# Kernel tuning notes

Hardware: AMD Instinct MI355X
Metric: run time of the kernel (lower is better)

Reference implementation:

```python
import jax, jax.numpy as jnp
import numpy as np

THRESH = 0.1  # Hardshrink lambda from init_kwargs


def setup_inputs() -> dict:
    key = jax.random.key(0)
    k1, k2, k3 = jax.random.split(key, 3)
    m, n, N = 64, 256, 131072
    phi = jax.random.normal(k1, (m, n), dtype=jnp.float32)
    X = jax.random.normal(k2, (n, N), dtype=jnp.float32)
    Y = jax.random.normal(k3, (m, N), dtype=jnp.float32)
    step = jnp.ones((1,), dtype=jnp.float32)  # learnable ISTA step size
    return {"phi": phi, "X": X, "Y": Y, "step": step, "idx": 100000}


def reference(phi, X, Y, step, idx):
    # The torch module updates column idx, then columns 0..idx-1, each with
    #   X[:, i] = hardshrink(X[:, i] + step * phi.T @ (Y[:, i] - phi @ X[:, i]))
    # (note: -(-1)*step == +step). Columns are independent and each column
    # reads only its own pre-update value, so the per-column loop is exactly
    # equivalent to two batched GEMMs over the prefix X[:, :idx+1] plus one
    # fused hard-threshold pass.
    k = idx + 1  # number of updated columns (idx is a static Python int)
    cols = X[:, :k]                       # [n, k]
    resid = Y[:, :k] - phi @ cols         # [m, k]
    upd = cols + step[0] * (phi.T @ resid)  # [n, k] gradient step
    upd = jnp.where(jnp.abs(upd) > THRESH, upd, jnp.zeros((), upd.dtype))
    X = X.at[:, :k].set(upd)
    return phi, X
```

## Files before the change

### kernel.cpp

```cpp
#include <hip/hip_runtime.h>
#include <math.h>

constexpr int M   = 64;
constexpr int NR  = 256;
constexpr int KK  = NR + M;
constexpr int NC  = 131072;
constexpr int BN  = 64;
constexpr float THR = 0.1f;

typedef __bf16 bf16x8 __attribute__((ext_vector_type(8)));
typedef float  f32x4  __attribute__((ext_vector_type(4)));

static __device__ __forceinline__ unsigned short f2bf(float f) {
    unsigned int u = __float_as_uint(f);
    u += 0x7FFFu + ((u >> 16) & 1u);
    return (unsigned short)(u >> 16);
}

__global__ __launch_bounds__(256)
void k_copy_phi(const float* __restrict__ phi, float* __restrict__ out)
{
    int i = blockIdx.x * 256 + threadIdx.x;
    out[i] = phi[i];
}

__global__ __launch_bounds__(256)
void k_prep(const float* __restrict__ phi, const float* __restrict__ step,
            unsigned short* __restrict__ A)
{
    __shared__ float ph[M * NR];
    const int i = blockIdx.x, j = threadIdx.x;
    for (int t = j; t < M * NR; t += 256) ph[t] = phi[t];
    __syncthreads();
    const float s = step[0];
    float d = 0.f;
    #pragma unroll
    for (int m = 0; m < M; ++m)
        d = fmaf(ph[m * NR + i], ph[m * NR + j], d);
    float w = ((i == j) ? 1.f : 0.f) - s * d;
    A[i * KK + j] = f2bf(w);
    if (j < M) A[i * KK + NR + j] = f2bf(s * ph[j * NR + i]);
}

__global__ __launch_bounds__(256, 3)
void k_gemm(const unsigned short* __restrict__ A,
            const float* __restrict__ X,
            const float* __restrict__ Y,
            const int*   __restrict__ idxp,
            float* __restrict__ outX)
{
    const int k   = idxp[0] + 1;
    const int n0  = blockIdx.x * BN;
    const int tid = threadIdx.x;

    if (n0 >= k) {
        const int c4 = tid & 15, rg = tid >> 4;
        #pragma unroll 4
        for (int r = rg; r < NR; r += 16) {
            const float4* src = (const float4*)(X + (size_t)r * NC + n0);
            float4*       dst = (float4*)(outX + (size_t)r * NC + n0);
            dst[c4] = src[c4];
        }
        return;
    }

    __shared__ unsigned int Bu32[10 * 2560 / 2];

    {
        const int n = tid & 63, slot = tid >> 6;
        for (int p = slot; p < KK / 2; p += 4) {
            const int r = p << 1;
            const float* s0 = (r < NR) ? (X + (size_t)r * NC)
                                       : (Y + (size_t)(r - NR) * NC);
            const float* s1 = (r < NR) ? (X + (size_t)(r + 1) * NC)
                                       : (Y + (size_t)(r + 1 - NR) * NC);
            float v0 = s0[n0 + n], v1 = s1[n0 + n];
            const int kb = r >> 5, kl = r & 31;
            Bu32[(kb * 2560 + n * 40 + kl) >> 1] =
                (unsigned int)f2bf(v0) | ((unsigned int)f2bf(v1) << 16);
        }
    }
    __syncthreads();

    const int lane = tid & 63, wave = tid >> 6;
    const int quad = lane >> 4, nlo = lane & 15;
    const int mbase = wave * 64;

    f32x4 acc[4][4];
    #pragma unroll
    for (int mt = 0; mt < 4; ++mt)
        #pragma unroll
        for (int nt = 0; nt < 4; ++nt)
            acc[mt][nt] = (f32x4){0.f, 0.f, 0.f, 0.f};

    const unsigned short* Abase = A + (size_t)(mbase + nlo) * KK + quad * 8;
    const unsigned int*   Bbase = Bu32 + ((nlo * 40 + quad * 8) >> 1);

    #pragma unroll 2
    for (int kb = 0; kb < 10; ++kb) {
        bf16x8 afr[4], bfr[4];
        #pragma unroll
        for (int mt = 0; mt < 4; ++mt)
            afr[mt] = *(const bf16x8*)(Abase + (size_t)mt * 16 * KK + kb * 32);
        #pragma unroll
        for (int nt = 0; nt < 4; ++nt)
            bfr[nt] = *(const bf16x8*)(Bbase + (kb * 2560 + nt * 16 * 40) / 2);
        #pragma unroll
        for (int mt = 0; mt < 4; ++mt)
            #pragma unroll
            for (int nt = 0; nt < 4; ++nt)
                acc[mt][nt] = __builtin_amdgcn_mfma_f32_16x16x32_bf16(
                    afr[mt], bfr[nt], acc[mt][nt], 0, 0, 0);
    }

    const bool boundary = (n0 + BN > k);
    #pragma unroll
    for (int mt = 0; mt < 4; ++mt) {
        #pragma unroll
        for (int nt = 0; nt < 4; ++nt) {
            const int col = n0 + nt * 16 + nlo;
            #pragma unroll
            for (int reg = 0; reg < 4; ++reg) {
                const int row = mbase + mt * 16 + quad * 4 + reg;
                float v = acc[mt][nt][reg];
                v = (fabsf(v) > THR) ? v : 0.f;
                if (boundary && col >= k) v = X[(size_t)row * NC + col];
                outX[(size_t)row * NC + col] = v;
            }
        }
    }
}

extern "C" void kernel_launch(void* const* d_in, const int* in_sizes, int n_in,
                              void* d_out, int out_size, void* d_ws, size_t ws_size,
                              hipStream_t stream)
{
    const float* phi  = (const float*)d_in[0];
    const float* X    = (const float*)d_in[1];
    const float* Y    = (const float*)d_in[2];
    const float* step = (const float*)d_in[3];
    const int*   idx  = (const int*)d_in[4];
    float* out = (float*)d_out;
    unsigned short* A = (unsigned short*)d_ws;

    k_copy_phi<<<(M * NR) / 256, 256, 0, stream>>>(phi, out);
    k_prep<<<NR, 256, 0, stream>>>(phi, step, A);
    k_gemm<<<NC / BN, 256, 0, stream>>>(A, X, Y, idx, out + M * NR);
}
```

Before: 322.9 us.

## Pre-swizzle A into fragment order, vectorize B staging, XOR-swizzle LDS, prefetch A

The prep kernel now writes the fused operator matrix in MFMA fragment order, so each lane loads contiguous 16-byte A fragments and the next k-block's A fragments can be prefetched into registers. B staging switches to float4 global loads that are held in registers and then written to an XOR-swizzled LDS layout, which is meant to avoid bank conflicts. The launch-bounds occupancy target rises from 3 to 4, and the copy loop is fully unrolled. The cost is higher register pressure from the 20 held float4 values plus the prefetched fragments, which may spill under the tighter occupancy bound.

Result: faster. 299.8 us (-7.1%).

```diff
diff --git a/kernel.cpp b/kernel.cpp
--- a/kernel.cpp
+++ b/kernel.cpp
@@ -15,6 +15,12 @@
     unsigned int u = __float_as_uint(f);
     u += 0x7FFFu + ((u >> 16) & 1u);
     return (unsigned short)(u >> 16);
+}
+
+static __device__ __forceinline__ int a_off(int i, int kk) {
+    const int wave = i >> 6, mt = (i >> 4) & 3, nlo = i & 15;
+    const int kb = kk >> 5, quad = (kk >> 3) & 3, j = kk & 7;
+    return (((wave * 10 + kb) * 4 + mt) << 9) + ((quad * 16 + nlo) << 3) + j;
 }
 
 __global__ __launch_bounds__(256)
@@ -38,11 +44,11 @@
     for (int m = 0; m < M; ++m)
         d = fmaf(ph[m * NR + i], ph[m * NR + j], d);
     float w = ((i == j) ? 1.f : 0.f) - s * d;
-    A[i * KK + j] = f2bf(w);
-    if (j < M) A[i * KK + NR + j] = f2bf(s * ph[j * NR + i]);
+    A[a_off(i, j)] = f2bf(w);
+    if (j < M) A[a_off(i, NR + j)] = f2bf(s * ph[j * NR + i]);
 }
 
-__global__ __launch_bounds__(256, 3)
+__global__ __launch_bounds__(256, 4)
 void k_gemm(const unsigned short* __restrict__ A,
             const float* __restrict__ X,
             const float* __restrict__ Y,
@@ -55,7 +61,7 @@
 
     if (n0 >= k) {
         const int c4 = tid & 15, rg = tid >> 4;
-        #pragma unroll 4
+        #pragma unroll
         for (int r = rg; r < NR; r += 16) {
             const float4* src = (const float4*)(X + (size_t)r * NC + n0);
             float4*       dst = (float4*)(outX + (size_t)r * NC + n0);
@@ -64,27 +70,41 @@
         return;
     }
 
-    __shared__ unsigned int Bu32[10 * 2560 / 2];
+    __shared__ unsigned int Bu32[10 * 4096 / 4];
 
-    {
-        const int n = tid & 63, slot = tid >> 6;
-        for (int p = slot; p < KK / 2; p += 4) {
-            const int r = p << 1;
-            const float* s0 = (r < NR) ? (X + (size_t)r * NC)
-                                       : (Y + (size_t)(r - NR) * NC);
-            const float* s1 = (r < NR) ? (X + (size_t)(r + 1) * NC)
-                                       : (Y + (size_t)(r + 1 - NR) * NC);
-            float v0 = s0[n0 + n], v1 = s1[n0 + n];
-            const int kb = r >> 5, kl = r & 31;
-            Bu32[(kb * 2560 + n * 40 + kl) >> 1] =
-                (unsigned int)f2bf(v0) | ((unsigned int)f2bf(v1) << 16);
+    const int c4 = tid & 15, rg = tid >> 4;
+    const int lane = tid & 63, wave = tid >> 6;
+    const int quad = lane >> 4, nlo = lane & 15;
+
+    f32x4 v0[10], v1[10];
+    #pragma unroll
+    for (int it = 0; it < 10; ++it) {
+        const int r0 = 32 * it + 2 * rg;
+        const float *s0, *s1;
+        if (r0 < NR) { s0 = X + (size_t)r0 * NC;        s1 = X + (size_t)(r0 + 1) * NC; }
+        else         { s0 = Y + (size_t)(r0 - NR) * NC; s1 = Y + (size_t)(r0 + 1 - NR) * NC; }
+        v0[it] = *(const f32x4*)(s0 + n0 + 4 * c4);
+        v1[it] = *(const f32x4*)(s1 + n0 + 4 * c4);
+    }
+
+    const unsigned short* Abase = A + ((wave * 40) << 9) + (lane << 3);
+    bf16x8 a_cur[4], a_nxt[4];
+    #pragma unroll
+    for (int mt = 0; mt < 4; ++mt)
+        a_cur[mt] = *(const bf16x8*)(Abase + (mt << 9));
+
+    #pragma unroll
+    for (int it = 0; it < 10; ++it) {
+        const int kl2 = 4 * rg;
+        #pragma unroll
+        for (int c = 0; c < 4; ++c) {
+            const int n = 4 * c4 + c;
+            const int byteoff = (it * 4096 + n * 64 + kl2) ^ ((n & 14) << 3);
+            Bu32[byteoff >> 2] =
+                (unsigned int)f2bf(v0[it][c]) | ((unsigned int)f2bf(v1[it][c]) << 16);
         }
     }
     __syncthreads();
-
-    const int lane = tid & 63, wave = tid >> 6;
-    const int quad = lane >> 4, nlo = lane & 15;
-    const int mbase = wave * 64;
 
     f32x4 acc[4][4];
     #pragma unroll
@@ -93,26 +113,31 @@
         for (int nt = 0; nt < 4; ++nt)
             acc[mt][nt] = (f32x4){0.f, 0.f, 0.f, 0.f};
 
-    const unsigned short* Abase = A + (size_t)(mbase + nlo) * KK + quad * 8;
-    const unsigned int*   Bbase = Bu32 + ((nlo * 40 + quad * 8) >> 1);
+    const char* Bbase = (const char*)Bu32 +
+                        (((unsigned)(nlo * 64 + quad * 16)) ^ ((nlo & 14) << 3));
 
-    #pragma unroll 2
+    #pragma unroll
     for (int kb = 0; kb < 10; ++kb) {
-        bf16x8 afr[4], bfr[4];
-        #pragma unroll
-        for (int mt = 0; mt < 4; ++mt)
-            afr[mt] = *(const bf16x8*)(Abase + (size_t)mt * 16 * KK + kb * 32);
+        if (kb < 9) {
+            #pragma unroll
+            for (int mt = 0; mt < 4; ++mt)
+                a_nxt[mt] = *(const bf16x8*)(Abase + (((kb + 1) * 4 + mt) << 9));
+        }
+        bf16x8 bfr[4];
         #pragma unroll
         for (int nt = 0; nt < 4; ++nt)
-            bfr[nt] = *(const bf16x8*)(Bbase + (kb * 2560 + nt * 16 * 40) / 2);
+            bfr[nt] = *(const bf16x8*)(Bbase + kb * 4096 + nt * 1024);
         #pragma unroll
         for (int mt = 0; mt < 4; ++mt)
             #pragma unroll
             for (int nt = 0; nt < 4; ++nt)
                 acc[mt][nt] = __builtin_amdgcn_mfma_f32_16x16x32_bf16(
-                    afr[mt], bfr[nt], acc[mt][nt], 0, 0, 0);
+                    a_cur[mt], bfr[nt], acc[mt][nt], 0, 0, 0);
+        #pragma unroll
+        for (int mt = 0; mt < 4; ++mt) a_cur[mt] = a_nxt[mt];
     }
 
+    const int mbase = wave * 64;
     const bool boundary = (n0 + BN > k);
     #pragma unroll
     for (int mt = 0; mt < 4; ++mt) {
```

## Pipeline B tiles via async global-to-LDS loads with larger 256-column blocks

Applied to the files above, without the earlier changes.

The GEMM kernel now processes 256 columns per block with 512 threads. It streams X/Y rows in K-chunks straight into LDS through global_load_lds, double-buffered, then converts them to bf16 into a swizzled LDS panel so the next chunk's load overlaps the MFMAs. The A matrix is pre-permuted into fragment order so each wave reads contiguous 16-byte fragments. Block IDs are remapped across the column space. The aim is to hide load latency and to cut per-element conversion and LDS bank conflicts, at the cost of 96KB of LDS per block, lower occupancy and fewer blocks.

Measured after the change: 287.3 us. 1.12x faster.

```diff
diff --git a/kernel.cpp b/kernel.cpp
--- a/kernel.cpp
+++ b/kernel.cpp
@@ -5,16 +5,43 @@
 constexpr int NR  = 256;
 constexpr int KK  = NR + M;
 constexpr int NC  = 131072;
-constexpr int BN  = 64;
+constexpr int BN  = 256;
+constexpr int GRID = NC / BN;
 constexpr float THR = 0.1f;
 
 typedef __bf16 bf16x8 __attribute__((ext_vector_type(8)));
 typedef float  f32x4  __attribute__((ext_vector_type(4)));
+typedef unsigned int u32;
 
 static __device__ __forceinline__ unsigned short f2bf(float f) {
     unsigned int u = __float_as_uint(f);
     u += 0x7FFFu + ((u >> 16) & 1u);
     return (unsigned short)(u >> 16);
+}
+
+static __device__ __forceinline__ void gload_lds16(const float* g, void* l) {
+    __builtin_amdgcn_global_load_lds(
+        (const __attribute__((address_space(1))) u32*)g,
+        (__attribute__((address_space(3))) u32*)l, 16, 0, 0);
+}
+template<int N> static __device__ __forceinline__ void waitv() {
+    asm volatile("s_waitcnt vmcnt(%0)" :: "i"(N));
+    __builtin_amdgcn_sched_barrier(0);
+}
+static __device__ __forceinline__ void waitl0() {
+    asm volatile("s_waitcnt lgkmcnt(0)" ::: "memory");
+    __builtin_amdgcn_sched_barrier(0);
+}
+static __device__ __forceinline__ void barrier_raw() {
+    asm volatile("" ::: "memory");
+    __builtin_amdgcn_s_barrier();
+    asm volatile("" ::: "memory");
+}
+
+static __device__ __forceinline__ int a_off(int i, int kk) {
+    const int wr = i >> 6, mt = (i >> 4) & 3, nlo = i & 15;
+    const int kb = kk >> 5, quad = (kk >> 3) & 3, j = kk & 7;
+    return (((wr * 10 + kb) * 4 + mt) << 9) + ((quad * 16 + nlo) << 3) + j;
 }
 
 __global__ __launch_bounds__(256)
@@ -38,11 +65,11 @@
     for (int m = 0; m < M; ++m)
         d = fmaf(ph[m * NR + i], ph[m * NR + j], d);
     float w = ((i == j) ? 1.f : 0.f) - s * d;
-    A[i * KK + j] = f2bf(w);
-    if (j < M) A[i * KK + NR + j] = f2bf(s * ph[j * NR + i]);
-}
-
-__global__ __launch_bounds__(256, 3)
+    A[a_off(i, j)] = f2bf(w);
+    if (j < M) A[a_off(i, NR + j)] = f2bf(s * ph[j * NR + i]);
+}
+
+__global__ __launch_bounds__(512)
 void k_gemm(const unsigned short* __restrict__ A,
             const float* __restrict__ X,
             const float* __restrict__ Y,
@@ -50,78 +77,104 @@
             float* __restrict__ outX)
 {
     const int k   = idxp[0] + 1;
-    const int n0  = blockIdx.x * BN;
+    const int bid = blockIdx.x;
+    const int n0  = ((bid & 7) * (GRID / 8) + (bid >> 3)) * BN;
     const int tid = threadIdx.x;
 
     if (n0 >= k) {
-        const int c4 = tid & 15, rg = tid >> 4;
-        #pragma unroll 4
-        for (int r = rg; r < NR; r += 16) {
-            const float4* src = (const float4*)(X + (size_t)r * NC + n0);
-            float4*       dst = (float4*)(outX + (size_t)r * NC + n0);
-            dst[c4] = src[c4];
+        for (int j = 0; j < 32; ++j) {
+            const int idx = tid + 512 * j;
+            const int r = idx >> 6, c4 = (idx & 63) * 4;
+            *(f32x4*)(outX + (size_t)r * NC + n0 + c4) =
+                *(const f32x4*)(X + (size_t)r * NC + n0 + c4);
         }
         return;
     }
 
-    __shared__ unsigned int Bu32[10 * 2560 / 2];
-
-    {
-        const int n = tid & 63, slot = tid >> 6;
-        for (int p = slot; p < KK / 2; p += 4) {
-            const int r = p << 1;
-            const float* s0 = (r < NR) ? (X + (size_t)r * NC)
-                                       : (Y + (size_t)(r - NR) * NC);
-            const float* s1 = (r < NR) ? (X + (size_t)(r + 1) * NC)
-                                       : (Y + (size_t)(r + 1 - NR) * NC);
-            float v0 = s0[n0 + n], v1 = s1[n0 + n];
-            const int kb = r >> 5, kl = r & 31;
-            Bu32[(kb * 2560 + n * 40 + kl) >> 1] =
-                (unsigned int)f2bf(v0) | ((unsigned int)f2bf(v1) << 16);
-        }
-    }
-    __syncthreads();
+    __shared__ __align__(16) unsigned char lds_raw[98304];
+    char* fpan = (char*)lds_raw;
+    char* bpan = (char*)lds_raw + 65536;
 
     const int lane = tid & 63, wave = tid >> 6;
+    const int wr = wave >> 1, wc = wave & 1;
     const int quad = lane >> 4, nlo = lane & 15;
-    const int mbase = wave * 64;
-
-    f32x4 acc[4][4];
+    const int rp = tid >> 5;
+    const int ca = (tid & 31) * 4;
+
+    auto issue = [&](int kb, int buf) {
+        #pragma unroll
+        for (int q = 0; q < 4; ++q) {
+            const int r  = wave * 4 + q;
+            const int gr = kb * 32 + r;
+            const float* src = (gr < NR ? X + (size_t)gr * NC
+                                        : Y + (size_t)(gr - NR) * NC) + n0;
+            gload_lds16(src + lane * 4, fpan + buf * 32768 + r * 1024);
+        }
+    };
+
+    issue(0, 0);
+
+    f32x4 acc[4][8];
     #pragma unroll
     for (int mt = 0; mt < 4; ++mt)
         #pragma unroll
-        for (int nt = 0; nt < 4; ++nt)
+        for (int nt = 0; nt < 8; ++nt)
             acc[mt][nt] = (f32x4){0.f, 0.f, 0.f, 0.f};
 
-    const unsigned short* Abase = A + (size_t)(mbase + nlo) * KK + quad * 8;
-    const unsigned int*   Bbase = Bu32 + ((nlo * 40 + quad * 8) >> 1);
+    const unsigned short* Abase = A + ((wr * 40) << 9) + (lane << 3);
+    const char* Bfrag = bpan + wc * 8192 +
+                        (((unsigned)(nlo * 64 + quad * 16)) ^ ((nlo & 14) << 3));
 
     #pragma unroll 2
     for (int kb = 0; kb < 10; ++kb) {
-        bf16x8 afr[4], bfr[4];
+        const int c = kb & 1;
+        waitv<0>();
+
+        bf16x8 afr[4];
         #pragma unroll
         for (int mt = 0; mt < 4; ++mt)
-            afr[mt] = *(const bf16x8*)(Abase + (size_t)mt * 16 * KK + kb * 32);
-        #pragma unroll
-        for (int nt = 0; nt < 4; ++nt)
-            bfr[nt] = *(const bf16x8*)(Bbase + (kb * 2560 + nt * 16 * 40) / 2);
-        #pragma unroll
-        for (int mt = 0; mt < 4; ++mt)
+            afr[mt] = *(const bf16x8*)(Abase + (((kb << 2) + mt) << 9));
+        __builtin_amdgcn_sched_barrier(0);
+
+        {
+            const char* fb = fpan + c * 32768 + (size_t)(2 * rp) * 1024;
+            f32x4 a0 = *(const f32x4*)(fb + ca * 4);
+            f32x4 a1 = *(const f32x4*)(fb + 1024 + ca * 4);
+            f32x4 b0 = *(const f32x4*)(fb + (ca + 128) * 4);
+            f32x4 b1 = *(const f32x4*)(fb + 1024 + (ca + 128) * 4);
+            char* bb = bpan + c * 16384;
             #pragma unroll
-            for (int nt = 0; nt < 4; ++nt)
+            for (int cc = 0; cc < 4; ++cc) {
+                const int n1 = ca + cc, n2 = n1 + 128;
+                const int o1 = (n1 * 64 + rp * 4) ^ ((n1 & 14) << 3);
+                const int o2 = (n2 * 64 + rp * 4) ^ ((n2 & 14) << 3);
+                *(u32*)(bb + o1) = (u32)f2bf(a0[cc]) | ((u32)f2bf(a1[cc]) << 16);
+                *(u32*)(bb + o2) = (u32)f2bf(b0[cc]) | ((u32)f2bf(b1[cc]) << 16);
+            }
+        }
+        waitl0();
+        if (kb < 9) issue(kb + 1, c ^ 1);
+        barrier_raw();
+
+        #pragma unroll
+        for (int nt = 0; nt < 8; ++nt) {
+            bf16x8 bfr = *(const bf16x8*)(Bfrag + c * 16384 + nt * 1024);
+            #pragma unroll
+            for (int mt = 0; mt < 4; ++mt)
                 acc[mt][nt] = __builtin_amdgcn_mfma_f32_16x16x32_bf16(
-                    afr[mt], bfr[nt], acc[mt][nt], 0, 0, 0);
+                    afr[mt], bfr, acc[mt][nt], 0, 0, 0);
+        }
     }
 
     const bool boundary = (n0 + BN > k);
     #pragma unroll
     for (int mt = 0; mt < 4; ++mt) {
         #pragma unroll
-        for (int nt = 0; nt < 4; ++nt) {
-            const int col = n0 + nt * 16 + nlo;
+        for (int nt = 0; nt < 8; ++nt) {
+            const int col = n0 + wc * 128 + nt * 16 + nlo;
             #pragma unroll
             for (int reg = 0; reg < 4; ++reg) {
-                const int row = mbase + mt * 16 + quad * 4 + reg;
+                const int row = wr * 64 + mt * 16 + quad * 4 + reg;
                 float v = acc[mt][nt][reg];
                 v = (fabsf(v) > THR) ? v : 0.f;
                 if (boundary && col >= k) v = X[(size_t)row * NC + col];
@@ -145,5 +198,5 @@
 
     k_copy_phi<<<(M * NR) / 256, 256, 0, stream>>>(phi, out);
     k_prep<<<NR, 256, 0, stream>>>(phi, step, A);
-    k_gemm<<<NC / BN, 256, 0, stream>>>(A, X, Y, idx, out + M * NR);
-}
+    k_gemm<<<GRID, 512, 0, stream>>>(A, X, Y, idx, out + M * NR);
+}
```
